# Optimization experiments

Hardware: AMD Instinct MI355X
Metric: run time of the kernel (lower is better)

Reference implementation:

```python
import jax, jax.numpy as jnp
import numpy as np

B, IN, U = 16, 1024, 1024


def _wSw(W, S):
    # W: [i,u], S: [b,i,i] -> W^T S W : [b,u,u]
    return jnp.einsum('iu,bij,jv->buv', W, S, W)


def _xSx(x, Wsig):
    # (sum_i x_i^2) * W_Sigma, broadcast over batch
    return jnp.sum(x * x, axis=1)[:, None, None] * Wsig


def _trS(S, Wsig):
    return jnp.trace(S, axis1=1, axis2=2)[:, None, None] * Wsig


def _hadamard_sigma(s1, s2, m1, m2):
    # s1*s2 + diag(m1) s2 diag(m1) + diag(m2) s1 diag(m2)
    return (s1 * s2
            + m1[:, :, None] * s2 * m1[:, None, :]
            + m2[:, :, None] * s1 * m2[:, None, :])


def _act_sigma(g, S):
    # S * outer(g, g)
    return S * (g[:, :, None] * g[:, None, :])


def setup_inputs() -> dict:
    key = jax.random.key(0)
    ks = jax.random.split(key, 16)
    f32 = jnp.float32
    init_mu, ini_sigma = 0.05, -4.6
    inp = {
        'mu_inputs': jax.random.normal(ks[0], (B, IN), f32),
        'sigma_inputs': 0.01 * jax.random.normal(ks[1], (B, IN, IN), f32),
        'prev_state': 0.1 * jax.random.normal(ks[2], (B, U), f32),
        'Sigma_state': 0.01 * jax.random.normal(ks[3], (B, U, U), f32),
        'U_z': init_mu * jax.random.normal(ks[4], (IN, U), f32),
        'uz_sigma': jnp.full((U,), ini_sigma, f32),
        'W_z': init_mu * jax.random.normal(ks[5], (U, U), f32),
        'wz_sigma': jnp.full((U,), ini_sigma, f32),
        'U_r': init_mu * jax.random.normal(ks[6], (IN, U), f32),
        'ur_sigma': jnp.full((U,), ini_sigma, f32),
        'W_r': init_mu * jax.random.normal(ks[7], (U, U), f32),
        'wr_sigma': jnp.full((U,), ini_sigma, f32),
        'U_h': init_mu * jax.random.normal(ks[8], (IN, U), f32),
        'uh_sigma': jnp.full((U,), ini_sigma, f32),
        'W_h': init_mu * jax.random.normal(ks[9], (U, U), f32),
        'wh_sigma': jnp.full((U,), ini_sigma, f32),
    }
    return inp


def reference(mu_inputs, sigma_inputs, prev_state, Sigma_state,
              U_z, uz_sigma, W_z, wz_sigma,
              U_r, ur_sigma, W_r, wr_sigma,
              U_h, uh_sigma, W_h, wh_sigma):
    sp = jax.nn.softplus
    # ---- z gate ----
    pre_z = mu_inputs @ U_z + prev_state @ W_z
    z = jax.nn.sigmoid(pre_z)
    Uz_S, Wz_S = jnp.diag(sp(uz_sigma)), jnp.diag(sp(wz_sigma))
    Sigma_zz = (_wSw(U_z, sigma_inputs) + _xSx(mu_inputs, Uz_S) + _trS(sigma_inputs, Uz_S)
                + _wSw(W_z, Sigma_state) + _xSx(prev_state, Wz_S) + _trS(Sigma_state, Wz_S))
    Sigma_z = _act_sigma(z * (1.0 - z), Sigma_zz)  # analytic d sigmoid
    # ---- r gate ----
    pre_r = mu_inputs @ U_r + prev_state @ W_r
    r = jax.nn.sigmoid(pre_r)
    Ur_S, Wr_S = jnp.diag(sp(ur_sigma)), jnp.diag(sp(wr_sigma))
    Sigma_rr = (_wSw(U_r, sigma_inputs) + _xSx(mu_inputs, Ur_S) + _trS(sigma_inputs, Ur_S)
                + _wSw(W_r, Sigma_state) + _xSx(prev_state, Wr_S) + _trS(Sigma_state, Wr_S))
    Sigma_r = _act_sigma(r * (1.0 - r), Sigma_rr)
    # ---- h gate ----
    sr = prev_state * r
    pre_h = mu_inputs @ U_h + sr @ W_h
    h = jnp.tanh(pre_h)
    Uh_S, Wh_S = jnp.diag(sp(uh_sigma)), jnp.diag(sp(wh_sigma))
    sigma_g = _hadamard_sigma(Sigma_state, Sigma_r, prev_state, r)
    Sigma_hh = (_wSw(U_h, sigma_inputs) + _xSx(mu_inputs, Uh_S) + _trS(sigma_inputs, Uh_S)
                + _wSw(W_h, sigma_g) + _xSx(sr, Wh_S) + _trS(sigma_g, Wh_S))
    Sigma_h = _act_sigma(1.0 - h * h, Sigma_hh)  # analytic d tanh
    # ---- combine ----
    mu_out = z * prev_state + (1.0 - z) * h
    sigma_a = _hadamard_sigma(Sigma_z, Sigma_state, z, prev_state)
    sigma_b = _hadamard_sigma(Sigma_z, Sigma_h, 1.0 - z, h)
    sigma_ab = Sigma_z * (prev_state[:, :, None] * h[:, None, :])
    sigma_abT = Sigma_z * (h[:, :, None] * prev_state[:, None, :])
    Sigma_out = sigma_a + sigma_b - sigma_ab - sigma_abT
    Sigma_out = jnp.where(jnp.isfinite(Sigma_out), Sigma_out, jnp.zeros_like(Sigma_out))
    eye = jnp.eye(Sigma_out.shape[-1], dtype=bool)
    Sigma_out = jnp.where(eye, jnp.abs(Sigma_out), Sigma_out)
    return mu_out, Sigma_out
```

## Files before the change

kernel.cpp:

```cpp
#include <hip/hip_runtime.h>
#include <math.h>


#define B_  16
#define N_  1024
#define NN_ (1024*1024)

typedef __bf16 bf16x8 __attribute__((ext_vector_type(8)));
typedef float  f32x4  __attribute__((ext_vector_type(4)));
typedef unsigned short ushort8v __attribute__((ext_vector_type(8)));

__device__ __forceinline__ unsigned short f2bf(float f) {
  union { float f; unsigned int u; } v; v.f = f;
  unsigned int r = v.u + 0x7fffu + ((v.u >> 16) & 1u);
  return (unsigned short)(r >> 16);
}
__device__ __forceinline__ float bf2f(unsigned short h) {
  union { unsigned int u; float f; } v; v.u = ((unsigned int)h) << 16;
  return v.f;
}
__device__ __forceinline__ float f4get(const float4& v, int q) {
  return q == 0 ? v.x : (q == 1 ? v.y : (q == 2 ? v.z : v.w));
}
__device__ __forceinline__ unsigned short u4get(const ushort4& v, int q) {
  return q == 0 ? v.x : (q == 1 ? v.y : (q == 2 ? v.z : v.w));
}

__device__ __forceinline__ void gload_lds16(const void* g, void* l) {
  __builtin_amdgcn_global_load_lds((__attribute__((address_space(1))) void*)g,
                                   (__attribute__((address_space(3))) void*)l,
                                   16, 0, 0);
}

template<int OMODE>
__global__ __launch_bounds__(512)
void gemm256(const unsigned short* __restrict__ A, int lda, long aStride, int koffA,
             const unsigned short* __restrict__ Bm, int ldb, long bStride,
             int K,
             void* __restrict__ Out, int ldo, long oStride, int noff,
             const float* __restrict__ act,
             const float* __restrict__ spU, const float* __restrict__ spW,
             const float* __restrict__ dU, const float* __restrict__ dW)
{
  __shared__ unsigned short lds[65536];
  const int b = blockIdx.z;
  const int nbase = blockIdx.x * 256;
  const int mbase = blockIdx.y * 256;
  const int t = threadIdx.x, lane = t & 63, w = t >> 6;
  const int wm = w >> 2, wn = w & 3;
  const int NT = K >> 5;

  f32x4 acc[8][4];
  const f32x4 zero4 = {0.f, 0.f, 0.f, 0.f};
#pragma unroll
  for (int i = 0; i < 8; i++)
#pragma unroll
    for (int j = 0; j < 4; j++) acc[i][j] = zero4;

  const int l3 = lane >> 3, l7 = lane & 7;
  const int posg = l7 ^ l3;
  const int gr = ((w * 8 + l3) << 1) + (posg >> 2);
  const int gc = (posg & 3) << 3;
  const unsigned short* Ag = A + (size_t)b * aStride + (size_t)(mbase + gr) * lda + koffA + gc;
  const unsigned short* Bg = Bm + (size_t)b * bStride + (size_t)(nbase + gr) * ldb + gc;
  const size_t a128 = (size_t)128 * lda, bb128 = (size_t)128 * ldb;
  char* ldsb = (char*)lds;
  const int wdst = w << 10;

  const int lrow = lane & 15, c4 = lane >> 4;
  const int aoff = ((lrow >> 1) << 7) + ((((((lrow & 1) << 2) | c4)) ^ (lrow >> 1)) << 4);
  const int abase0 = (wm << 13);
  const int bbase0 = 16384 + (wn << 12);

  auto STAGE = [&](int kt) {
    const int p = kt & 3;
    const size_t ko = (size_t)kt << 5;
    char* base = ldsb + (p << 15);
    gload_lds16(Ag + ko,          base + wdst);
    gload_lds16(Ag + ko + a128,   base + 8192  + wdst);
    gload_lds16(Bg + ko,          base + 16384 + wdst);
    gload_lds16(Bg + ko + bb128,  base + 24576 + wdst);
  };

  STAGE(0); STAGE(1);
  asm volatile("s_waitcnt vmcnt(4)" ::: "memory");
  __builtin_amdgcn_sched_barrier(0);
  __builtin_amdgcn_s_barrier();
  __builtin_amdgcn_sched_barrier(0);

  for (int kt = 0; kt < NT; ++kt) {
    if (kt + 2 < NT) STAGE(kt + 2);
    const char* pbuf = ldsb + ((size_t)(kt & 3) << 15);
    bf16x8 av[8], bv[4];
#pragma unroll
    for (int mi = 0; mi < 8; mi++)
      av[mi] = *(const bf16x8*)(pbuf + abase0 + (mi << 10) + aoff);
#pragma unroll
    for (int ni = 0; ni < 4; ni++)
      bv[ni] = *(const bf16x8*)(pbuf + bbase0 + (ni << 10) + aoff);
#pragma unroll
    for (int ni = 0; ni < 4; ni++)
#pragma unroll
      for (int mi = 0; mi < 8; mi++)
        acc[mi][ni] = __builtin_amdgcn_mfma_f32_16x16x32_bf16(av[mi], bv[ni], acc[mi][ni], 0, 0, 0);
    if (kt + 1 < NT) {
      if (kt + 2 < NT) asm volatile("s_waitcnt vmcnt(4)" ::: "memory");
      else             asm volatile("s_waitcnt vmcnt(0)" ::: "memory");
      __builtin_amdgcn_sched_barrier(0);
      __builtin_amdgcn_s_barrier();
      __builtin_amdgcn_sched_barrier(0);
    }
  }

  if (OMODE == 2) {
    const float* actb = act + b * N_;
    const float dUb = dU[b], dWb = dW[b];
#pragma unroll
    for (int mi = 0; mi < 8; mi++) {
      const int u0 = mbase + wm * 128 + mi * 16 + ((lane >> 4) << 2);
#pragma unroll
      for (int ni = 0; ni < 4; ni++) {
        const int v = nbase + wn * 64 + ni * 16 + (lane & 15);
        const float avv = actb[v];
#pragma unroll
        for (int r = 0; r < 4; r++) {
          const int u = u0 + r;
          float val = acc[mi][ni][r];
          if (u == v) val += dUb * spU[u] + dWb * spW[u];
          val *= actb[u] * avv;
          ((float*)Out)[(size_t)b * oStride + (size_t)u * ldo + v] = val;
        }
      }
    }
  } else {
    __syncthreads();
    unsigned short* reg = lds + w * 8192;
    const float* actb = (OMODE == 1) ? (act + b * N_) : nullptr;
    float dUb = 0.f, dWb = 0.f;
    if (OMODE == 1) { dUb = dU[b]; dWb = dW[b]; }
#pragma unroll
    for (int mi = 0; mi < 8; mi++) {
      const int rl0 = mi * 16 + ((lane >> 4) << 2);
#pragma unroll
      for (int ni = 0; ni < 4; ni++) {
        const int cl = ni * 16 + (lane & 15);
#pragma unroll
        for (int r = 0; r < 4; r++) {
          const int rl = rl0 + r;
          float val = acc[mi][ni][r];
          if (OMODE == 1) {
            const int u = mbase + wm * 128 + rl, v = nbase + wn * 64 + cl;
            if (u == v) val += dUb * spU[u] + dWb * spW[u];
            val *= actb[u] * actb[v];
          }
          reg[rl * 64 + cl] = f2bf(val);
        }
      }
    }
    unsigned short* obase = (unsigned short*)Out + (size_t)b * oStride
        + (size_t)(mbase + wm * 128) * ldo + noff + nbase + wn * 64;
#pragma unroll
    for (int pp = 0; pp < 16; pp++) {
      const int row = pp * 8 + (lane >> 3);
      const int ch = lane & 7;
      ushort8v vv = *(const ushort8v*)&reg[row * 64 + ch * 8];
      *(ushort8v*)(obase + (size_t)row * ldo + ch * 8) = vv;
    }
  }
}


__global__ void conv_bf16(const float* __restrict__ in, unsigned short* __restrict__ out, int n4)
{
  int i = blockIdx.x * 256 + threadIdx.x;
  const int stride = gridDim.x * 256;
  for (; i < n4; i += stride) {
    const float4 v = ((const float4*)in)[i];
    ushort4 o;
    o.x = f2bf(v.x); o.y = f2bf(v.y); o.z = f2bf(v.z); o.w = f2bf(v.w);
    ((ushort4*)out)[i] = o;
  }
}

__global__ void build_AT(const float* __restrict__ Uz, const float* __restrict__ Wz,
                         const float* __restrict__ Ur, const float* __restrict__ Wr,
                         const float* __restrict__ Uh, const float* __restrict__ Wh,
                         unsigned short* __restrict__ AT)
{
  __shared__ float tile[32][33];
  const int g = blockIdx.z;
  const float* U = g == 0 ? Uz : (g == 1 ? Ur : Uh);
  const float* W = g == 0 ? Wz : (g == 1 ? Wr : Wh);
  const int u0  = blockIdx.x * 32;
  const int k0g = blockIdx.y * 32;
  const float* src = (k0g >= 1024) ? W : U;
  const int kloc = k0g & 1023;
  const int tx = threadIdx.x & 31, ty = threadIdx.x >> 5;
  unsigned short* out = AT + (size_t)g * N_ * 2048;
#pragma unroll
  for (int i = 0; i < 32; i += 8) tile[ty + i][tx] = src[(size_t)(kloc + ty + i) * N_ + u0 + tx];
  __syncthreads();
#pragma unroll
  for (int i = 0; i < 32; i += 8)
    out[(size_t)(u0 + ty + i) * 2048 + k0g + tx] = f2bf(tile[tx][ty + i]);
}

__global__ void softplus6(const float* a0, const float* a1, const float* a2,
                          const float* a3, const float* a4, const float* a5,
                          float* __restrict__ sp)
{
  const float* src[6] = {a0, a1, a2, a3, a4, a5};
  const int g = blockIdx.x;
  const float* s = src[g];
  for (int i = threadIdx.x; i < N_; i += 256) {
    float x = s[i];
    sp[g * N_ + i] = (x > 20.f) ? x : log1pf(expf(x));
  }
}

__global__ void scalars1(const float* __restrict__ mu, const float* __restrict__ prev,
                         const float* __restrict__ sin_, const float* __restrict__ Sst,
                         float* __restrict__ dA, float* __restrict__ dBzr)
{
  __shared__ float red[256];
  const int b = blockIdx.x;
  float s1 = 0.f, s2 = 0.f;
  for (int i = threadIdx.x; i < N_; i += 256) {
    const float m = mu[b * N_ + i];
    s1 += m * m + sin_[(size_t)b * NN_ + (size_t)i * (N_ + 1)];
    const float p = prev[b * N_ + i];
    s2 += p * p + Sst[(size_t)b * NN_ + (size_t)i * (N_ + 1)];
  }
  red[threadIdx.x] = s1; __syncthreads();
  for (int s = 128; s > 0; s >>= 1) { if (threadIdx.x < s) red[threadIdx.x] += red[threadIdx.x + s]; __syncthreads(); }
  if (threadIdx.x == 0) dA[b] = red[0];
  __syncthreads();
  red[threadIdx.x] = s2; __syncthreads();
  for (int s = 128; s > 0; s >>= 1) { if (threadIdx.x < s) red[threadIdx.x] += red[threadIdx.x + s]; __syncthreads(); }
  if (threadIdx.x == 0) dBzr[b] = red[0];
}

__global__ __launch_bounds__(256)
void gate_pre2(const float* __restrict__ x1, const float* __restrict__ x2,
               const float* __restrict__ U0, const float* __restrict__ W0,
               const float* __restrict__ U1, const float* __restrict__ W1,
               float* __restrict__ Ppart)
{
  const int g  = blockIdx.z;
  const int ks = blockIdx.y;
  const int out = blockIdx.x * 256 + threadIdx.x;
  const int b = out >> 10, col = out & 1023;
  const float* x = (ks < 4) ? x1 : x2;
  const float* Wm = (g == 0) ? ((ks < 4) ? U0 : W0) : ((ks < 4) ? U1 : W1);
  const int k0 = (ks & 3) * 256;
  const float* xb = x + b * N_ + k0;
  const float* wp = Wm + (size_t)k0 * N_ + col;
  float acc = 0.f;
#pragma unroll 8
  for (int k = 0; k < 256; k++)
    acc += xb[k] * wp[(size_t)k * N_];
  Ppart[(g * 8 + ks) * (B_ * N_) + out] = acc;
}

__global__ void gate_act2(const float* __restrict__ P,
                          float* __restrict__ z, float* __restrict__ gz,
                          float* __restrict__ r, float* __restrict__ gr)
{
  const int out = blockIdx.x * 256 + threadIdx.x;
  float a0 = 0.f, a1 = 0.f;
#pragma unroll
  for (int ks = 0; ks < 8; ks++) {
    a0 += P[ks * (B_ * N_) + out];
    a1 += P[(8 + ks) * (B_ * N_) + out];
  }
  const float s0 = 1.f / (1.f + expf(-a0));
  const float s1 = 1.f / (1.f + expf(-a1));
  z[out] = s0; gz[out] = s0 * (1.f - s0);
  r[out] = s1; gr[out] = s1 * (1.f - s1);
}

__global__ __launch_bounds__(256)
void gate_pre1(const float* __restrict__ x1, const float* __restrict__ x2,
               const float* __restrict__ U0, const float* __restrict__ W0,
               float* __restrict__ Ppart)
{
  const int ks = blockIdx.y;
  const int out = blockIdx.x * 256 + threadIdx.x;
  const int b = out >> 10, col = out & 1023;
  const float* x = (ks < 4) ? x1 : x2;
  const float* Wm = (ks < 4) ? U0 : W0;
  const int k0 = (ks & 3) * 256;
  const float* xb = x + b * N_ + k0;
  const float* wp = Wm + (size_t)k0 * N_ + col;
  float acc = 0.f;
#pragma unroll 8
  for (int k = 0; k < 256; k++)
    acc += xb[k] * wp[(size_t)k * N_];
  Ppart[ks * (B_ * N_) + out] = acc;
}

__global__ void gate_act1(const float* __restrict__ P,
                          float* __restrict__ h, float* __restrict__ gh)
{
  const int out = blockIdx.x * 256 + threadIdx.x;
  float a0 = 0.f;
#pragma unroll
  for (int ks = 0; ks < 8; ks++) a0 += P[ks * (B_ * N_) + out];
  const float s = tanhf(a0);
  h[out] = s; gh[out] = 1.f - s * s;
}

__global__ void sr_csr(const float* __restrict__ prev, const float* __restrict__ r,
                       float* __restrict__ sr, float* __restrict__ csr)
{
  __shared__ float red[256];
  const int b = blockIdx.x;
  float s = 0.f;
  for (int i = threadIdx.x; i < N_; i += 256) {
    const float v = prev[b * N_ + i] * r[b * N_ + i];
    sr[b * N_ + i] = v;
    s += v * v;
  }
  red[threadIdx.x] = s; __syncthreads();
  for (int k = 128; k > 0; k >>= 1) { if (threadIdx.x < k) red[threadIdx.x] += red[threadIdx.x + k]; __syncthreads(); }
  if (threadIdx.x == 0) csr[b] = red[0];
}

__global__ void hadamard_sg(const float* __restrict__ Sst, unsigned short* __restrict__ Sg,
                            const float* __restrict__ prev, const float* __restrict__ r)
{
  const size_t idx = ((size_t)blockIdx.x * 256 + threadIdx.x) * 4;
  const int b = (int)(idx >> 20);
  const int rem = (int)(idx & (NN_ - 1));
  const int i = rem >> 10, j0 = rem & 1023;
  const float pi = prev[b * N_ + i], ri = r[b * N_ + i];
  const float4  ss  = *(const float4*)(Sst + (size_t)b * NN_ + rem);
  const ushort4 sr4 = *(const ushort4*)(Sg + (size_t)b * NN_ + rem);
  ushort4 o;
  unsigned short* op = (unsigned short*)&o;
#pragma unroll
  for (int q = 0; q < 4; q++) {
    const float srv = bf2f(u4get(sr4, q));
    const float stv = f4get(ss, q);
    const float pj = prev[b * N_ + j0 + q];
    const float rj = r[b * N_ + j0 + q];
    op[q] = f2bf(stv * srv + pi * pj * srv + ri * rj * stv);
  }
  *(ushort4*)(Sg + (size_t)b * NN_ + rem) = o;
}

__global__ void scalars2(const unsigned short* __restrict__ Sg,
                         const float* __restrict__ csr, float* __restrict__ dBh)
{
  __shared__ float red[256];
  const int b = blockIdx.x;
  float s = 0.f;
  for (int i = threadIdx.x; i < N_; i += 256)
    s += bf2f(Sg[(size_t)b * NN_ + (size_t)i * (N_ + 1)]);
  red[threadIdx.x] = s; __syncthreads();
  for (int k = 128; k > 0; k >>= 1) { if (threadIdx.x < k) red[threadIdx.x] += red[threadIdx.x + k]; __syncthreads(); }
  if (threadIdx.x == 0) dBh[b] = red[0] + csr[b];
}

__global__ void mu_kernel(const float* __restrict__ z, const float* __restrict__ prev,
                          const float* __restrict__ h, float* __restrict__ mu_out)
{
  const int i = blockIdx.x * 256 + threadIdx.x;
  const float zz = z[i];
  mu_out[i] = zz * prev[i] + (1.f - zz) * h[i];
}

__global__ void combine(const unsigned short* __restrict__ Sz, const float* __restrict__ Sst,
                        const float* __restrict__ z, const float* __restrict__ prev,
                        const float* __restrict__ h, float* __restrict__ SigOut)
{
  const int row = blockIdx.x;
  const int b = row >> 10, u = row & 1023;
  const float zu = z[b * N_ + u], pu = prev[b * N_ + u], hu = h[b * N_ + u];
  const size_t base = (size_t)b * NN_ + (size_t)u * N_;
  const int j0 = threadIdx.x * 4;
  const ushort4 s4 = *(const ushort4*)(Sz + base + j0);
  const float4 sh = *(const float4*)(SigOut + base + j0);
  const float4 st = *(const float4*)(Sst + base + j0);
  const float4 zv = *(const float4*)(z + b * N_ + j0);
  const float4 pv = *(const float4*)(prev + b * N_ + j0);
  const float4 hv = *(const float4*)(h + b * N_ + j0);
  float o[4];
#pragma unroll
  for (int q = 0; q < 4; q++) {
    const int v = j0 + q;
    const float sz  = bf2f(u4get(s4, q));
    const float shh = f4get(sh, q);
    const float stt = f4get(st, q);
    const float zvv = f4get(zv, q);
    const float pvv = f4get(pv, q);
    const float hvv = f4get(hv, q);
    float res = sz * stt + zu * zvv * stt + pu * pvv * sz
              + sz * shh + (1.f - zu) * (1.f - zvv) * shh + hu * hvv * sz
              - sz * (pu * hvv) - sz * (hu * pvv);
    if (!isfinite(res)) res = 0.f;
    if (u == v) res = fabsf(res);
    o[q] = res;
  }
  float4 ov; ov.x = o[0]; ov.y = o[1]; ov.z = o[2]; ov.w = o[3];
  *(float4*)(SigOut + base + j0) = ov;
}


extern "C" void kernel_launch(void* const* d_in, const int* in_sizes, int n_in,
                              void* d_out, int out_size, void* d_ws, size_t ws_size,
                              hipStream_t stream)
{
  const float* mu   = (const float*)d_in[0];
  const float* sin_ = (const float*)d_in[1];
  const float* prev = (const float*)d_in[2];
  const float* Sst  = (const float*)d_in[3];
  const float* Uz = (const float*)d_in[4];  const float* uzs = (const float*)d_in[5];
  const float* Wz = (const float*)d_in[6];  const float* wzs = (const float*)d_in[7];
  const float* Ur = (const float*)d_in[8];  const float* urs = (const float*)d_in[9];
  const float* Wr = (const float*)d_in[10]; const float* wrs = (const float*)d_in[11];
  const float* Uh = (const float*)d_in[12]; const float* uhs = (const float*)d_in[13];
  const float* Wh = (const float*)d_in[14]; const float* whs = (const float*)d_in[15];

  char* ws = (char*)d_ws;
  size_t off = 0;
  auto take = [&](size_t bytes) -> char* {
    char* p = ws + off;
    off = (off + bytes + 255) & ~(size_t)255;
    return p;
  };
  unsigned short* Tcm = (unsigned short*)take((size_t)B_ * 2048 * 1024 * 2);
  unsigned short* Sz  = (unsigned short*)take((size_t)B_ * NN_ * 2);
  unsigned short* Sg  = (unsigned short*)take((size_t)B_ * NN_ * 2);
  unsigned short* AT  = (unsigned short*)take((size_t)3 * N_ * 2048 * 2);
  float* Ppart = (float*)take((size_t)16 * B_ * N_ * 4);
  float* sp   = (float*)take(6 * N_ * 4);
  float* z    = (float*)take(B_ * N_ * 4);
  float* gz   = (float*)take(B_ * N_ * 4);
  float* rr   = (float*)take(B_ * N_ * 4);
  float* gr   = (float*)take(B_ * N_ * 4);
  float* h    = (float*)take(B_ * N_ * 4);
  float* gh   = (float*)take(B_ * N_ * 4);
  float* sr   = (float*)take(B_ * N_ * 4);
  float* dA   = (float*)take(64);
  float* dBzr = (float*)take(64);
  float* dBh  = (float*)take(64);
  float* csr  = (float*)take(64);
  if (off > ws_size) return;

  float* mu_out = (float*)d_out;
  float* SigOut = (float*)d_out + (size_t)B_ * N_;
  unsigned short* SinH = (unsigned short*)SigOut;
  unsigned short* SstH = (unsigned short*)SigOut + (size_t)B_ * NN_;

  const unsigned short* ATz = AT;
  const unsigned short* ATr = AT + (size_t)N_ * 2048;
  const unsigned short* ATh = AT + (size_t)2 * N_ * 2048;

  conv_bf16<<<2048, 256, 0, stream>>>(sin_, SinH, B_ * NN_ / 4);
  conv_bf16<<<2048, 256, 0, stream>>>(Sst,  SstH, B_ * NN_ / 4);
  softplus6<<<6, 256, 0, stream>>>(uzs, wzs, urs, wrs, uhs, whs, sp);
  scalars1<<<16, 256, 0, stream>>>(mu, prev, sin_, Sst, dA, dBzr);
  build_AT<<<dim3(32, 64, 3), 256, 0, stream>>>(Uz, Wz, Ur, Wr, Uh, Wh, AT);
  gate_pre2<<<dim3(64, 8, 2), 256, 0, stream>>>(mu, prev, Uz, Wz, Ur, Wr, Ppart);
  gate_act2<<<64, 256, 0, stream>>>(Ppart, z, gz, rr, gr);
  sr_csr<<<16, 256, 0, stream>>>(prev, rr, sr, csr);
  gate_pre1<<<dim3(64, 8), 256, 0, stream>>>(mu, sr, Uh, Wh, Ppart);
  gate_act1<<<64, 256, 0, stream>>>(Ppart, h, gh);

  const dim3 gg(4, 4, 16);
  const long tS = (long)2048 * 1024;

  gemm256<0><<<gg, 512, 0, stream>>>(ATz, 2048, 0, 0,    SinH, 1024, (long)NN_, 1024,
                                     Tcm, 2048, tS, 0,    nullptr, nullptr, nullptr, nullptr, nullptr);
  gemm256<0><<<gg, 512, 0, stream>>>(ATz, 2048, 0, 1024, SstH, 1024, (long)NN_, 1024,
                                     Tcm, 2048, tS, 1024, nullptr, nullptr, nullptr, nullptr, nullptr);
  gemm256<1><<<gg, 512, 0, stream>>>(ATz, 2048, 0, 0,    Tcm, 2048, tS, 2048,
                                     Sz, 1024, (long)NN_, 0, gz, sp + 0, sp + 1024, dA, dBzr);
  gemm256<0><<<gg, 512, 0, stream>>>(ATr, 2048, 0, 0,    SinH, 1024, (long)NN_, 1024,
                                     Tcm, 2048, tS, 0,    nullptr, nullptr, nullptr, nullptr, nullptr);
  gemm256<0><<<gg, 512, 0, stream>>>(ATr, 2048, 0, 1024, SstH, 1024, (long)NN_, 1024,
                                     Tcm, 2048, tS, 1024, nullptr, nullptr, nullptr, nullptr, nullptr);
  gemm256<1><<<gg, 512, 0, stream>>>(ATr, 2048, 0, 0,    Tcm, 2048, tS, 2048,
                                     Sg, 1024, (long)NN_, 0, gr, sp + 2048, sp + 3072, dA, dBzr);
  hadamard_sg<<<16384, 256, 0, stream>>>(Sst, Sg, prev, rr);
  scalars2<<<16, 256, 0, stream>>>(Sg, csr, dBh);
  gemm256<0><<<gg, 512, 0, stream>>>(ATh, 2048, 0, 0,    SinH, 1024, (long)NN_, 1024,
                                     Tcm, 2048, tS, 0,    nullptr, nullptr, nullptr, nullptr, nullptr);
  gemm256<0><<<gg, 512, 0, stream>>>(ATh, 2048, 0, 1024, Sg,   1024, (long)NN_, 1024,
                                     Tcm, 2048, tS, 1024, nullptr, nullptr, nullptr, nullptr, nullptr);
  gemm256<2><<<gg, 512, 0, stream>>>(ATh, 2048, 0, 0,    Tcm, 2048, tS, 2048,
                                     SigOut, 1024, (long)NN_, 0, gh, sp + 4096, sp + 5120, dA, dBh);
  mu_kernel<<<64, 256, 0, stream>>>(z, prev, h, mu_out);
  combine<<<16384, 256, 0, stream>>>(Sz, Sst, z, prev, h, SigOut);
}
```

Baseline: 590.6 us.

## Shrink GEMM tiles to 128x256, pair first-stage GEMMs, add XCD-aware block mapping

Replaces the 256x256-tile batched GEMM with a 128x256-tile variant. It uses a double-buffered 48KB LDS pipeline and launch bounds that allow more resident blocks. The two first-stage GEMMs per gate, over sigma_inputs and the state covariance, are merged into one launch, and a 1D grid is remapped so tiles sharing data land on the same XCD. The epilogue staging buffer is XOR-swizzled to cut LDS bank conflicts. Smaller tiles and double rather than quad buffering raise occupancy and parallelism but reduce per-block reuse and pipeline depth.

```diff
diff --git a/kernel.cpp b/kernel.cpp
--- a/kernel.cpp
+++ b/kernel.cpp
@@ -32,28 +32,37 @@
                                    16, 0, 0);
 }
 
-template<int OMODE>
-__global__ __launch_bounds__(512)
-void gemm256(const unsigned short* __restrict__ A, int lda, long aStride, int koffA,
-             const unsigned short* __restrict__ Bm, int ldb, long bStride,
-             int K,
-             void* __restrict__ Out, int ldo, long oStride, int noff,
-             const float* __restrict__ act,
-             const float* __restrict__ spU, const float* __restrict__ spW,
-             const float* __restrict__ dU, const float* __restrict__ dW)
-{
-  __shared__ unsigned short lds[65536];
-  const int b = blockIdx.z;
-  const int nbase = blockIdx.x * 256;
-  const int mbase = blockIdx.y * 256;
+template<int OMODE, int PAIR>
+__global__ __launch_bounds__(512, 4)
+void gemmT(const unsigned short* __restrict__ A, int lda, long aStride, int koffA,
+           const unsigned short* __restrict__ Bm, const unsigned short* __restrict__ Bm2,
+           int ldb, long bStride, int K,
+           void* __restrict__ Out, int ldo, long oStride, int noff,
+           const float* __restrict__ act,
+           const float* __restrict__ spU, const float* __restrict__ spW,
+           const float* __restrict__ dU, const float* __restrict__ dW)
+{
+  __shared__ __align__(16) char ldsb[49152];
+  const int id  = blockIdx.x;
+  const int xcd = id & 7, loc = id >> 3;
+  const int mt  = loc & 7;
+  const int pidx = xcd + ((loc >> 3) << 3);
+  const int nt  = pidx & 3;
+  const int b   = (pidx >> 2) & 15;
+  const int ps  = PAIR ? (pidx >> 6) : 0;
+  const unsigned short* Bsel = (PAIR && ps) ? Bm2 : Bm;
+  const int kofx = koffA + (ps ? 1024 : 0);
+  const int nofx = noff  + (ps ? 1024 : 0);
+  const int mbase = mt << 7;
+  const int nbase = nt << 8;
   const int t = threadIdx.x, lane = t & 63, w = t >> 6;
   const int wm = w >> 2, wn = w & 3;
   const int NT = K >> 5;
 
-  f32x4 acc[8][4];
+  f32x4 acc[4][4];
   const f32x4 zero4 = {0.f, 0.f, 0.f, 0.f};
 #pragma unroll
-  for (int i = 0; i < 8; i++)
+  for (int i = 0; i < 4; i++)
 #pragma unroll
     for (int j = 0; j < 4; j++) acc[i][j] = zero4;
 
@@ -61,39 +70,39 @@
   const int posg = l7 ^ l3;
   const int gr = ((w * 8 + l3) << 1) + (posg >> 2);
   const int gc = (posg & 3) << 3;
-  const unsigned short* Ag = A + (size_t)b * aStride + (size_t)(mbase + gr) * lda + koffA + gc;
-  const unsigned short* Bg = Bm + (size_t)b * bStride + (size_t)(nbase + gr) * ldb + gc;
-  const size_t a128 = (size_t)128 * lda, bb128 = (size_t)128 * ldb;
-  char* ldsb = (char*)lds;
+  const unsigned short* Ag = A + (size_t)b * aStride + (size_t)(mbase + gr) * lda + kofx + gc;
+  const unsigned short* Bg = Bsel + (size_t)b * bStride + (size_t)(nbase + gr) * ldb + gc;
+  const size_t b128s = (size_t)128 * ldb;
   const int wdst = w << 10;
 
   const int lrow = lane & 15, c4 = lane >> 4;
-  const int aoff = ((lrow >> 1) << 7) + ((((((lrow & 1) << 2) | c4)) ^ (lrow >> 1)) << 4);
-  const int abase0 = (wm << 13);
-  const int bbase0 = 16384 + (wn << 12);
+  const int aoff = ((lrow >> 1) << 7) + (((((lrow & 1) << 2) | c4) ^ (lrow >> 1)) << 4);
+  const int abase0 = wm << 12;
+  const int bbase0 = 8192 + (wn << 12);
 
   auto STAGE = [&](int kt) {
-    const int p = kt & 3;
+    char* base = ldsb + (kt & 1) * 24576;
     const size_t ko = (size_t)kt << 5;
-    char* base = ldsb + (p << 15);
-    gload_lds16(Ag + ko,          base + wdst);
-    gload_lds16(Ag + ko + a128,   base + 8192  + wdst);
-    gload_lds16(Bg + ko,          base + 16384 + wdst);
-    gload_lds16(Bg + ko + bb128,  base + 24576 + wdst);
+    gload_lds16(Ag + ko,         base + wdst);
+    gload_lds16(Bg + ko,         base + 8192  + wdst);
+    gload_lds16(Bg + ko + b128s, base + 16384 + wdst);
   };
 
-  STAGE(0); STAGE(1);
-  asm volatile("s_waitcnt vmcnt(4)" ::: "memory");
-  __builtin_amdgcn_sched_barrier(0);
-  __builtin_amdgcn_s_barrier();
-  __builtin_amdgcn_sched_barrier(0);
-
+  STAGE(0);
   for (int kt = 0; kt < NT; ++kt) {
-    if (kt + 2 < NT) STAGE(kt + 2);
-    const char* pbuf = ldsb + ((size_t)(kt & 3) << 15);
-    bf16x8 av[8], bv[4];
-#pragma unroll
-    for (int mi = 0; mi < 8; mi++)
+    if (kt + 1 < NT) {
+      STAGE(kt + 1);
+      asm volatile("s_waitcnt vmcnt(3)" ::: "memory");
+    } else {
+      asm volatile("s_waitcnt vmcnt(0)" ::: "memory");
+    }
+    __builtin_amdgcn_sched_barrier(0);
+    __builtin_amdgcn_s_barrier();
+    __builtin_amdgcn_sched_barrier(0);
+    const char* pbuf = ldsb + (kt & 1) * 24576;
+    bf16x8 av[4], bv[4];
+#pragma unroll
+    for (int mi = 0; mi < 4; mi++)
       av[mi] = *(const bf16x8*)(pbuf + abase0 + (mi << 10) + aoff);
 #pragma unroll
     for (int ni = 0; ni < 4; ni++)
@@ -101,23 +110,19 @@
 #pragma unroll
     for (int ni = 0; ni < 4; ni++)
 #pragma unroll
-      for (int mi = 0; mi < 8; mi++)
+      for (int mi = 0; mi < 4; mi++)
         acc[mi][ni] = __builtin_amdgcn_mfma_f32_16x16x32_bf16(av[mi], bv[ni], acc[mi][ni], 0, 0, 0);
-    if (kt + 1 < NT) {
-      if (kt + 2 < NT) asm volatile("s_waitcnt vmcnt(4)" ::: "memory");
-      else             asm volatile("s_waitcnt vmcnt(0)" ::: "memory");
-      __builtin_amdgcn_sched_barrier(0);
-      __builtin_amdgcn_s_barrier();
-      __builtin_amdgcn_sched_barrier(0);
-    }
+    __builtin_amdgcn_sched_barrier(0);
+    __builtin_amdgcn_s_barrier();
+    __builtin_amdgcn_sched_barrier(0);
   }
 
   if (OMODE == 2) {
     const float* actb = act + b * N_;
     const float dUb = dU[b], dWb = dW[b];
 #pragma unroll
-    for (int mi = 0; mi < 8; mi++) {
-      const int u0 = mbase + wm * 128 + mi * 16 + ((lane >> 4) << 2);
+    for (int mi = 0; mi < 4; mi++) {
+      const int u0 = mbase + wm * 64 + mi * 16 + ((lane >> 4) << 2);
 #pragma unroll
       for (int ni = 0; ni < 4; ni++) {
         const int v = nbase + wn * 64 + ni * 16 + (lane & 15);
@@ -134,37 +139,47 @@
     }
   } else {
     __syncthreads();
-    unsigned short* reg = lds + w * 8192;
+    unsigned short* scr = (unsigned short*)(ldsb + w * 4096);
     const float* actb = (OMODE == 1) ? (act + b * N_) : nullptr;
     float dUb = 0.f, dWb = 0.f;
     if (OMODE == 1) { dUb = dU[b]; dWb = dW[b]; }
 #pragma unroll
-    for (int mi = 0; mi < 8; mi++) {
-      const int rl0 = mi * 16 + ((lane >> 4) << 2);
-#pragma unroll
-      for (int ni = 0; ni < 4; ni++) {
-        const int cl = ni * 16 + (lane & 15);
-#pragma unroll
-        for (int r = 0; r < 4; r++) {
-          const int rl = rl0 + r;
-          float val = acc[mi][ni][r];
-          if (OMODE == 1) {
-            const int u = mbase + wm * 128 + rl, v = nbase + wn * 64 + cl;
-            if (u == v) val += dUb * spU[u] + dWb * spW[u];
-            val *= actb[u] * actb[v];
+    for (int p = 0; p < 2; ++p) {
+#pragma unroll
+      for (int mi = 2 * p; mi < 2 * p + 2; ++mi) {
+        const int rl0 = (mi - 2 * p) * 16 + ((lane >> 4) << 2);
+#pragma unroll
+        for (int ni = 0; ni < 4; ni++) {
+          const int cl = ni * 16 + (lane & 15);
+#pragma unroll
+          for (int r = 0; r < 4; r++) {
+            const int rl = rl0 + r;
+            float val = acc[mi][ni][r];
+            if (OMODE == 1) {
+              const int u = mbase + wm * 64 + mi * 16 + ((lane >> 4) << 2) + r;
+              const int v = nbase + wn * 64 + cl;
+              if (u == v) val += dUb * spU[u] + dWb * spW[u];
+              val *= actb[u] * actb[v];
+            }
+            scr[rl * 64 + ((((cl >> 3) ^ (rl & 7))) << 3) + (cl & 7)] = f2bf(val);
           }
-          reg[rl * 64 + cl] = f2bf(val);
         }
       }
-    }
-    unsigned short* obase = (unsigned short*)Out + (size_t)b * oStride
-        + (size_t)(mbase + wm * 128) * ldo + noff + nbase + wn * 64;
-#pragma unroll
-    for (int pp = 0; pp < 16; pp++) {
-      const int row = pp * 8 + (lane >> 3);
-      const int ch = lane & 7;
-      ushort8v vv = *(const ushort8v*)&reg[row * 64 + ch * 8];
-      *(ushort8v*)(obase + (size_t)row * ldo + ch * 8) = vv;
+      asm volatile("s_waitcnt lgkmcnt(0)" ::: "memory");
+      __builtin_amdgcn_sched_barrier(0);
+      unsigned short* ob = (unsigned short*)Out + (size_t)b * oStride
+          + (size_t)(mbase + wm * 64 + p * 32) * ldo + nofx + nbase + wn * 64;
+#pragma unroll
+      for (int pp = 0; pp < 4; pp++) {
+        const int row = pp * 8 + (lane >> 3);
+        const int ch = (lane & 7) ^ (row & 7);
+        ushort8v vv = *(const ushort8v*)&scr[row * 64 + ((lane & 7) << 3)];
+        *(ushort8v*)(ob + (size_t)row * ldo + ch * 8) = vv;
+      }
+      if (p == 0) {
+        asm volatile("s_waitcnt lgkmcnt(0)" ::: "memory");
+        __builtin_amdgcn_sched_barrier(0);
+      }
     }
   }
 }
@@ -468,29 +483,22 @@
   gate_pre1<<<dim3(64, 8), 256, 0, stream>>>(mu, sr, Uh, Wh, Ppart);
   gate_act1<<<64, 256, 0, stream>>>(Ppart, h, gh);
 
-  const dim3 gg(4, 4, 16);
   const long tS = (long)2048 * 1024;
 
-  gemm256<0><<<gg, 512, 0, stream>>>(ATz, 2048, 0, 0,    SinH, 1024, (long)NN_, 1024,
-                                     Tcm, 2048, tS, 0,    nullptr, nullptr, nullptr, nullptr, nullptr);
-  gemm256<0><<<gg, 512, 0, stream>>>(ATz, 2048, 0, 1024, SstH, 1024, (long)NN_, 1024,
-                                     Tcm, 2048, tS, 1024, nullptr, nullptr, nullptr, nullptr, nullptr);
-  gemm256<1><<<gg, 512, 0, stream>>>(ATz, 2048, 0, 0,    Tcm, 2048, tS, 2048,
-                                     Sz, 1024, (long)NN_, 0, gz, sp + 0, sp + 1024, dA, dBzr);
-  gemm256<0><<<gg, 512, 0, stream>>>(ATr, 2048, 0, 0,    SinH, 1024, (long)NN_, 1024,
-                                     Tcm, 2048, tS, 0,    nullptr, nullptr, nullptr, nullptr, nullptr);
-  gemm256<0><<<gg, 512, 0, stream>>>(ATr, 2048, 0, 1024, SstH, 1024, (long)NN_, 1024,
-                                     Tcm, 2048, tS, 1024, nullptr, nullptr, nullptr, nullptr, nullptr);
-  gemm256<1><<<gg, 512, 0, stream>>>(ATr, 2048, 0, 0,    Tcm, 2048, tS, 2048,
-                                     Sg, 1024, (long)NN_, 0, gr, sp + 2048, sp + 3072, dA, dBzr);
+  gemmT<0, 1><<<1024, 512, 0, stream>>>(ATz, 2048, 0, 0, SinH, SstH, 1024, (long)NN_, 1024,
+                                        Tcm, 2048, tS, 0, nullptr, nullptr, nullptr, nullptr, nullptr);
+  gemmT<1, 0><<<512, 512, 0, stream>>>(ATz, 2048, 0, 0, Tcm, nullptr, 2048, tS, 2048,
+                                       Sz, 1024, (long)NN_, 0, gz, sp + 0, sp + 1024, dA, dBzr);
+  gemmT<0, 1><<<1024, 512, 0, stream>>>(ATr, 2048, 0, 0, SinH, SstH, 1024, (long)NN_, 1024,
+                                        Tcm, 2048, tS, 0, nullptr, nullptr, nullptr, nullptr, nullptr);
+  gemmT<1, 0><<<512, 512, 0, stream>>>(ATr, 2048, 0, 0, Tcm, nullptr, 2048, tS, 2048,
+                                       Sg, 1024, (long)NN_, 0, gr, sp + 2048, sp + 3072, dA, dBzr);
   hadamard_sg<<<16384, 256, 0, stream>>>(Sst, Sg, prev, rr);
   scalars2<<<16, 256, 0, stream>>>(Sg, csr, dBh);
-  gemm256<0><<<gg, 512, 0, stream>>>(ATh, 2048, 0, 0,    SinH, 1024, (long)NN_, 1024,
-                                     Tcm, 2048, tS, 0,    nullptr, nullptr, nullptr, nullptr, nullptr);
-  gemm256<0><<<gg, 512, 0, stream>>>(ATh, 2048, 0, 1024, Sg,   1024, (long)NN_, 1024,
-                                     Tcm, 2048, tS, 1024, nullptr, nullptr, nullptr, nullptr, nullptr);
-  gemm256<2><<<gg, 512, 0, stream>>>(ATh, 2048, 0, 0,    Tcm, 2048, tS, 2048,
-                                     SigOut, 1024, (long)NN_, 0, gh, sp + 4096, sp + 5120, dA, dBh);
+  gemmT<0, 1><<<1024, 512, 0, stream>>>(ATh, 2048, 0, 0, SinH, Sg, 1024, (long)NN_, 1024,
+                                        Tcm, 2048, tS, 0, nullptr, nullptr, nullptr, nullptr, nullptr);
+  gemmT<2, 0><<<512, 512, 0, stream>>>(ATh, 2048, 0, 0, Tcm, nullptr, 2048, tS, 2048,
+                                       SigOut, 1024, (long)NN_, 0, gh, sp + 4096, sp + 5120, dA, dBh);
   mu_kernel<<<64, 256, 0, stream>>>(z, prev, h, mu_out);
   combine<<<16384, 256, 0, stream>>>(Sz, Sst, z, prev, h, SigOut);
 }
```

New measurement: 612.7 us. +3.7%, slower.
